# Performance work log

Measured on AMD Instinct MI355X. Metric: run time of the kernel, lower is better.

The kernel has to match this reference:

```python
import jax, jax.numpy as jnp
import numpy as np

N_EMBD = 1024
N_HEAD = 16
HEAD_DIM = N_EMBD // N_HEAD


def setup_inputs() -> dict:
    key = jax.random.key(0)
    ks = jax.random.split(key, 5)
    B, T, C = 4, 2048, N_EMBD
    x = jax.random.normal(ks[0], (B, T, C), dtype=jnp.float32)
    # torch Linear: y = x @ W.T + b; store W in [out, in] like torch
    scale = 1.0 / np.sqrt(C)
    W_attn = jax.random.normal(ks[1], (3 * C, C), dtype=jnp.float32) * scale
    b_attn = jnp.zeros((3 * C,), dtype=jnp.float32)
    W_proj = jax.random.normal(ks[2], (C, C), dtype=jnp.float32) * scale
    b_proj = jnp.zeros((C,), dtype=jnp.float32)
    return {"x": x, "W_attn": W_attn, "b_attn": b_attn, "W_proj": W_proj, "b_proj": b_proj}


def reference(x, W_attn, b_attn, W_proj, b_proj):
    B, T, C = x.shape
    H, D = N_HEAD, HEAD_DIM
    qkv = x @ W_attn.T + b_attn                    # [B,T,3C]
    q, k, v = jnp.split(qkv, 3, axis=-1)
    q = q.reshape(B, T, H, D).transpose(0, 2, 1, 3)  # [B,H,T,D]
    k = k.reshape(B, T, H, D).transpose(0, 2, 1, 3)
    v = v.reshape(B, T, H, D).transpose(0, 2, 1, 3)
    att = jnp.einsum('bhtd,bhsd->bhts', q, k) / jnp.sqrt(jnp.float32(D))  # [B,H,T,T]
    causal = jnp.tril(jnp.ones((T, T), dtype=bool))
    att = jnp.where(causal[None, None], att, -jnp.inf)
    att = jax.nn.softmax(att, axis=-1)
    # dropout is identity in eval mode (pdrop=0.0)
    y = jnp.einsum('bhts,bhsd->bhtd', att, v)      # [B,H,T,D]
    y = y.transpose(0, 2, 1, 3).reshape(B, T, C)
    return y @ W_proj.T + b_proj
```

## Files before the change

### kernel.cpp

```cpp
#include <hip/hip_runtime.h>
#include <stdint.h>


#define SEQ 2048
#define NBATCH 4
#define CEMB 1024
#define NHEAD 16
#define DHEAD 64
#define BTROWS (NBATCH * SEQ)

typedef __bf16 bf16x8 __attribute__((ext_vector_type(8)));
typedef float f32x4 __attribute__((ext_vector_type(4)));
typedef float f32x16 __attribute__((ext_vector_type(16)));
typedef uint32_t u32x4 __attribute__((ext_vector_type(4)));
typedef unsigned short u16;

__device__ __forceinline__ u16 f2bf(float f) {
  union { float f; uint32_t u; } x; x.f = f;
  uint32_t u = x.u;
  return (u16)((u + 0x7FFFu + ((u >> 16) & 1u)) >> 16);
}

__device__ __forceinline__ uint32_t pk2(float a, float b) {
  union { __bf16 h[2]; uint32_t u; } z;
  z.h[0] = (__bf16)a; z.h[1] = (__bf16)b;
  return z.u;
}

__device__ __forceinline__ void gload_lds16(const void* g, void* l) {
  __builtin_amdgcn_global_load_lds(
      (const __attribute__((address_space(1))) uint32_t*)g,
      (__attribute__((address_space(3))) uint32_t*)l, 16, 0, 0);
}

__global__ __launch_bounds__(256) void cvt_f32_bf16_kernel(
    const float* __restrict__ in, u16* __restrict__ out, int n4) {
  int i = blockIdx.x * blockDim.x + threadIdx.x;
  int stride = gridDim.x * blockDim.x;
  for (; i < n4; i += stride) {
    float4 v = reinterpret_cast<const float4*>(in)[i];
    ushort4 o;
    o.x = f2bf(v.x); o.y = f2bf(v.y); o.z = f2bf(v.z); o.w = f2bf(v.w);
    reinterpret_cast<ushort4*>(out)[i] = o;
  }
}

template <bool OUT_BF16>
__global__ __launch_bounds__(256) void gemm_bt_kernel(
    const u16* __restrict__ A, const u16* __restrict__ Bt,
    const float* __restrict__ bias, void* __restrict__ Cout,
    int M, int N, int K) {
  __shared__ u16 As[128][64];
  __shared__ u16 Bs[128][64];
  const int tid = threadIdx.x;
  const int lane = tid & 63;
  const int wave = tid >> 6;
  const int wr = wave >> 1, wc = wave & 1;
  const int m0 = blockIdx.y * 128;
  const int n0 = blockIdx.x * 128;
  const int l15 = lane & 15, lhi = lane >> 4;

  f32x4 acc[4][4];
#pragma unroll
  for (int i = 0; i < 4; i++)
#pragma unroll
    for (int j = 0; j < 4; j++) acc[i][j] = (f32x4){0.f, 0.f, 0.f, 0.f};

  const int srow = lane >> 3;
  const int scol = (lane & 7) * 8;

  for (int kt = 0; kt < K; kt += 64) {
#pragma unroll
    for (int i = 0; i < 4; i++) {
      int rr = (wave * 4 + i) * 8 + srow;
      gload_lds16(A + (size_t)(m0 + rr) * K + kt + scol, &As[(wave * 4 + i) * 8][0]);
      gload_lds16(Bt + (size_t)(n0 + rr) * K + kt + scol, &Bs[(wave * 4 + i) * 8][0]);
    }
    __syncthreads();
#pragma unroll
    for (int ks = 0; ks < 2; ks++) {
      bf16x8 af[4], bfr[4];
#pragma unroll
      for (int mi = 0; mi < 4; mi++)
        af[mi] = *(const bf16x8*)&As[wr * 64 + mi * 16 + l15][ks * 32 + lhi * 8];
#pragma unroll
      for (int ni = 0; ni < 4; ni++)
        bfr[ni] = *(const bf16x8*)&Bs[wc * 64 + ni * 16 + l15][ks * 32 + lhi * 8];
#pragma unroll
      for (int mi = 0; mi < 4; mi++)
#pragma unroll
        for (int ni = 0; ni < 4; ni++)
          acc[mi][ni] = __builtin_amdgcn_mfma_f32_16x16x32_bf16(
              af[mi], bfr[ni], acc[mi][ni], 0, 0, 0);
    }
    __syncthreads();
  }

#pragma unroll
  for (int mi = 0; mi < 4; mi++) {
#pragma unroll
    for (int ni = 0; ni < 4; ni++) {
      int n = n0 + wc * 64 + ni * 16 + l15;
      float bv = bias[n];
#pragma unroll
      for (int r = 0; r < 4; r++) {
        int m = m0 + wr * 64 + mi * 16 + lhi * 4 + r;
        float v = acc[mi][ni][r] + bv;
        if constexpr (OUT_BF16)
          ((u16*)Cout)[(size_t)m * N + n] = f2bf(v);
        else
          ((float*)Cout)[(size_t)m * N + n] = v;
      }
    }
  }
}

__global__ __launch_bounds__(256) void attn_kernel(
    const u16* __restrict__ qkv, u16* __restrict__ yatt) {
  __shared__ u16 Ks[64][64];
  __shared__ u16 Vt[64][68];

  const int tid = threadIdx.x;
  const int lane = tid & 63;
  const int wave = tid >> 6;
  const int qt = 15 - (int)blockIdx.x;
  const int bh = blockIdx.y;
  const int b = bh >> 4, h = bh & 15;
  const int l31 = lane & 31, hi = lane >> 5;

  const size_t rs = 3 * CEMB;
  const u16* qb = qkv + (size_t)b * SEQ * rs + h * DHEAD;
  const u16* kb = qb + CEMB;
  const u16* vb = qb + 2 * CEMB;

  const int q0 = qt * 128;
  const int qabs = q0 + wave * 32 + l31;

  bf16x8 qf[4];
  {
    const u16* qp = qb + (size_t)qabs * rs + hi * 8;
#pragma unroll
    for (int dc = 0; dc < 4; dc++) qf[dc] = *(const bf16x8*)(qp + dc * 16);
  }

  float m_acc = -1e30f, l_acc = 0.f;
  f32x16 o_acc[2];
  o_acc[0] = (f32x16)(0.f);
  o_acc[1] = (f32x16)(0.f);

  const float SCLL2E = 0.125f * 1.44269504088896f;

  for (int s0 = 0; s0 <= q0 + 64; s0 += 64) {
#pragma unroll
    for (int c = 0; c < 2; c++) {
      int row0 = (c * 4 + wave) * 8;
      int row = row0 + (lane >> 3);
      int cb = (lane & 7) ^ (row & 7);
      gload_lds16(kb + (size_t)(s0 + row) * rs + cb * 8, &Ks[row0][0]);
    }
    {
      const u16* gv = vb + (size_t)(s0 + lane) * rs + wave * 16;
      union { u32x4 q[2]; u16 u[16]; } tv;
      tv.q[0] = *(const u32x4*)gv;
      tv.q[1] = *(const u32x4*)(gv + 8);
#pragma unroll
      for (int j = 0; j < 16; j++) Vt[wave * 16 + j][lane] = tv.u[j];
    }
    __syncthreads();

    const bool active = (s0 <= q0 + wave * 32 + 31);
    if (active) {
      f32x16 sf[2];
#pragma unroll
      for (int kt = 0; kt < 2; kt++) {
        f32x16 s = (f32x16)(0.f);
        int key = kt * 32 + l31;
#pragma unroll
        for (int dc = 0; dc < 4; dc++) {
          int cb = (dc * 2 + hi) ^ (key & 7);
          const bf16x8 kf = *(const bf16x8*)((const u16*)&Ks[key][0] + cb * 8);
          s = __builtin_amdgcn_mfma_f32_32x32x16_bf16(kf, qf[dc], s, 0, 0, 0);
        }
        sf[kt] = s;
      }

      if (s0 + 63 > q0 + wave * 32) {
#pragma unroll
        for (int kt = 0; kt < 2; kt++)
#pragma unroll
          for (int r = 0; r < 16; r++) {
            int key = s0 + kt * 32 + (r & 3) + 8 * (r >> 2) + 4 * hi;
            if (key > qabs) sf[kt][r] = -3e38f;
          }
      }

      float cmax = sf[0][0];
#pragma unroll
      for (int r = 1; r < 16; r++) cmax = fmaxf(cmax, sf[0][r]);
#pragma unroll
      for (int r = 0; r < 16; r++) cmax = fmaxf(cmax, sf[1][r]);
      cmax = fmaxf(cmax, __shfl_xor(cmax, 32, 64));

      if (!__all(cmax <= m_acc + 64.0f)) {
        float mnew = fmaxf(m_acc, cmax);
        float scf = __builtin_amdgcn_exp2f((m_acc - mnew) * SCLL2E);
        m_acc = mnew;
        l_acc *= scf;
        float scr[16];
#pragma unroll
        for (int r = 0; r < 16; r++)
          scr[r] = __shfl(scf, (r & 3) + 8 * (r >> 2) + 4 * hi, 64);
#pragma unroll
        for (int r = 0; r < 16; r++) {
          o_acc[0][r] *= scr[r];
          o_acc[1][r] *= scr[r];
        }
      }

      const float c1 = -m_acc * SCLL2E;
      float ps = 0.f;
#pragma unroll
      for (int kt = 0; kt < 2; kt++)
#pragma unroll
        for (int r = 0; r < 16; r++) {
          float p = __builtin_amdgcn_exp2f(fmaf(sf[kt][r], SCLL2E, c1));
          sf[kt][r] = p;
          ps += p;
        }
      ps += __shfl_xor(ps, 32, 64);
      l_acc += ps;

      bf16x8 pa[4];
#pragma unroll
      for (int ks = 0; ks < 4; ks++) {
        const int t = ks >> 1;
        const int ra = (ks & 1) * 8;
        uint32_t a  = pk2(sf[t][ra + 0], sf[t][ra + 1]);
        uint32_t b2 = pk2(sf[t][ra + 2], sf[t][ra + 3]);
        uint32_t cc = pk2(sf[t][ra + 4], sf[t][ra + 5]);
        uint32_t dd = pk2(sf[t][ra + 6], sf[t][ra + 7]);
        uint32_t snd0 = hi ? a : cc;
        uint32_t snd1 = hi ? b2 : dd;
        uint32_t r0 = __shfl_xor(snd0, 32, 64);
        uint32_t r1 = __shfl_xor(snd1, 32, 64);
        union { bf16x8 v; uint32_t w[4]; } u;
        u.w[0] = hi ? r0 : a;
        u.w[1] = hi ? r1 : b2;
        u.w[2] = hi ? cc : r0;
        u.w[3] = hi ? dd : r1;
        pa[ks] = u.v;
      }

#pragma unroll
      for (int dt = 0; dt < 2; dt++) {
        const u16* vrow = &Vt[dt * 32 + l31][hi * 8];
#pragma unroll
        for (int ks = 0; ks < 4; ks++) {
          union { bf16x8 v; uint2 d[2]; } u;
          u.d[0] = *(const uint2*)(vrow + ks * 16);
          u.d[1] = *(const uint2*)(vrow + ks * 16 + 4);
          o_acc[dt] = __builtin_amdgcn_mfma_f32_32x32x16_bf16(pa[ks], u.v, o_acc[dt], 0, 0, 0);
        }
      }
    }
    __syncthreads();
  }

  float rl = 1.0f / l_acc;
#pragma unroll
  for (int r = 0; r < 16; r++) {
    int crow = (r & 3) + 8 * (r >> 2) + 4 * hi;
    float linv = __shfl(rl, crow, 64);
    int t = q0 + wave * 32 + crow;
    u16* yp = yatt + ((size_t)(b * SEQ + t)) * CEMB + h * DHEAD + l31;
    yp[0]  = f2bf(o_acc[0][r] * linv);
    yp[32] = f2bf(o_acc[1][r] * linv);
  }
}

extern "C" void kernel_launch(void* const* d_in, const int* in_sizes, int n_in,
                              void* d_out, int out_size, void* d_ws, size_t ws_size,
                              hipStream_t stream) {
  const float* x      = (const float*)d_in[0];
  const float* W_attn = (const float*)d_in[1];
  const float* b_attn = (const float*)d_in[2];
  const float* W_proj = (const float*)d_in[3];
  const float* b_proj = (const float*)d_in[4];
  float* out = (float*)d_out;

  u16* Xb   = (u16*)d_ws;
  u16* Wab  = Xb  + (size_t)BTROWS * CEMB;
  u16* Wpb  = Wab + (size_t)3 * CEMB * CEMB;
  u16* QKV  = Wpb + (size_t)CEMB * CEMB;
  u16* Yatt = QKV + (size_t)BTROWS * 3 * CEMB;

  cvt_f32_bf16_kernel<<<2048, 256, 0, stream>>>(x, Xb, BTROWS * CEMB / 4);
  cvt_f32_bf16_kernel<<<1024, 256, 0, stream>>>(W_attn, Wab, 3 * CEMB * CEMB / 4);
  cvt_f32_bf16_kernel<<<512, 256, 0, stream>>>(W_proj, Wpb, CEMB * CEMB / 4);

  gemm_bt_kernel<true><<<dim3(3 * CEMB / 128, BTROWS / 128), 256, 0, stream>>>(
      Xb, Wab, b_attn, QKV, BTROWS, 3 * CEMB, CEMB);

  attn_kernel<<<dim3(SEQ / 128, NBATCH * NHEAD), 256, 0, stream>>>(QKV, Yatt);

  gemm_bt_kernel<false><<<dim3(CEMB / 128, BTROWS / 128), 256, 0, stream>>>(
      Yatt, Wpb, b_proj, out, BTROWS, CEMB, CEMB);
}
```

Baseline: 339.1 us.

## Pair causal query tiles per block and widen attention key tiles to 128

Each attention block now handles two query tiles, p and 15-p, one after the other. This balances the causal workload across blocks and halves the grid. The key/value tile grows from 64 to 128 keys per iteration, which halves the barrier count and lets the masking apply only to the diagonal tile. It also adds s_setprio around the MFMA sections and tree reductions for the row max and sum. The cost is more LDS and registers per block and fewer blocks in flight, which could hurt occupancy.

Result: faster. 331.1 us (-2.4%).

```diff
diff --git a/kernel.cpp b/kernel.cpp
--- a/kernel.cpp
+++ b/kernel.cpp
@@ -117,13 +117,13 @@
 
 __global__ __launch_bounds__(256) void attn_kernel(
     const u16* __restrict__ qkv, u16* __restrict__ yatt) {
-  __shared__ u16 Ks[64][64];
-  __shared__ u16 Vt[64][68];
+  __shared__ u16 Ks[128][64];
+  __shared__ u16 Vt[64][132];
 
   const int tid = threadIdx.x;
   const int lane = tid & 63;
   const int wave = tid >> 6;
-  const int qt = 15 - (int)blockIdx.x;
+  const int p = blockIdx.x;
   const int bh = blockIdx.y;
   const int b = bh >> 4, h = bh & 15;
   const int l31 = lane & 31, hi = lane >> 5;
@@ -133,46 +133,48 @@
   const u16* kb = qb + CEMB;
   const u16* vb = qb + 2 * CEMB;
 
-  const int q0 = qt * 128;
-  const int qabs = q0 + wave * 32 + l31;
-
-  bf16x8 qf[4];
-  {
-    const u16* qp = qb + (size_t)qabs * rs + hi * 8;
-#pragma unroll
-    for (int dc = 0; dc < 4; dc++) qf[dc] = *(const bf16x8*)(qp + dc * 16);
-  }
-
-  float m_acc = -1e30f, l_acc = 0.f;
-  f32x16 o_acc[2];
-  o_acc[0] = (f32x16)(0.f);
-  o_acc[1] = (f32x16)(0.f);
-
   const float SCLL2E = 0.125f * 1.44269504088896f;
 
-  for (int s0 = 0; s0 <= q0 + 64; s0 += 64) {
-#pragma unroll
-    for (int c = 0; c < 2; c++) {
-      int row0 = (c * 4 + wave) * 8;
-      int row = row0 + (lane >> 3);
-      int cb = (lane & 7) ^ (row & 7);
-      gload_lds16(kb + (size_t)(s0 + row) * rs + cb * 8, &Ks[row0][0]);
-    }
+  for (int pass = 0; pass < 2; ++pass) {
+    const int qt = pass ? (15 - p) : p;
+    const int q0 = qt * 128;
+    const int qabs = q0 + wave * 32 + l31;
+
+    bf16x8 qf[4];
     {
-      const u16* gv = vb + (size_t)(s0 + lane) * rs + wave * 16;
-      union { u32x4 q[2]; u16 u[16]; } tv;
-      tv.q[0] = *(const u32x4*)gv;
-      tv.q[1] = *(const u32x4*)(gv + 8);
-#pragma unroll
-      for (int j = 0; j < 16; j++) Vt[wave * 16 + j][lane] = tv.u[j];
-    }
-    __syncthreads();
-
-    const bool active = (s0 <= q0 + wave * 32 + 31);
-    if (active) {
-      f32x16 sf[2];
-#pragma unroll
-      for (int kt = 0; kt < 2; kt++) {
+      const u16* qp = qb + (size_t)qabs * rs + hi * 8;
+#pragma unroll
+      for (int dc = 0; dc < 4; dc++) qf[dc] = *(const bf16x8*)(qp + dc * 16);
+    }
+
+    float m_acc = -1e30f, l_acc = 0.f;
+    f32x16 o_acc[2];
+    o_acc[0] = (f32x16)(0.f);
+    o_acc[1] = (f32x16)(0.f);
+
+    for (int s0 = 0; s0 <= q0; s0 += 128) {
+#pragma unroll
+      for (int c = 0; c < 4; c++) {
+        int row0 = (c * 4 + wave) * 8;
+        int row = row0 + (lane >> 3);
+        int cb = (lane & 7) ^ (row & 7);
+        gload_lds16(kb + (size_t)(s0 + row) * rs + cb * 8, &Ks[row0][0]);
+      }
+#pragma unroll
+      for (int half = 0; half < 2; ++half) {
+        const u16* gv = vb + (size_t)(s0 + half * 64 + lane) * rs + wave * 16;
+        union { u32x4 q[2]; u16 u[16]; } tv;
+        tv.q[0] = *(const u32x4*)gv;
+        tv.q[1] = *(const u32x4*)(gv + 8);
+#pragma unroll
+        for (int j = 0; j < 16; j++) Vt[wave * 16 + j][half * 64 + lane] = tv.u[j];
+      }
+      __syncthreads();
+
+      f32x16 sf[4];
+      __builtin_amdgcn_s_setprio(1);
+#pragma unroll
+      for (int kt = 0; kt < 4; kt++) {
         f32x16 s = (f32x16)(0.f);
         int key = kt * 32 + l31;
 #pragma unroll
@@ -183,10 +185,11 @@
         }
         sf[kt] = s;
       }
-
-      if (s0 + 63 > q0 + wave * 32) {
-#pragma unroll
-        for (int kt = 0; kt < 2; kt++)
+      __builtin_amdgcn_s_setprio(0);
+
+      if (s0 == q0) {
+#pragma unroll
+        for (int kt = 0; kt < 4; kt++)
 #pragma unroll
           for (int r = 0; r < 16; r++) {
             int key = s0 + kt * 32 + (r & 3) + 8 * (r >> 2) + 4 * hi;
@@ -194,11 +197,15 @@
           }
       }
 
-      float cmax = sf[0][0];
-#pragma unroll
-      for (int r = 1; r < 16; r++) cmax = fmaxf(cmax, sf[0][r]);
-#pragma unroll
-      for (int r = 0; r < 16; r++) cmax = fmaxf(cmax, sf[1][r]);
+      float t16[16];
+#pragma unroll
+      for (int i = 0; i < 16; i++)
+        t16[i] = fmaxf(fmaxf(sf[0][i], sf[1][i]), fmaxf(sf[2][i], sf[3][i]));
+#pragma unroll
+      for (int i = 0; i < 8; i++) t16[i] = fmaxf(t16[i], t16[i + 8]);
+#pragma unroll
+      for (int i = 0; i < 4; i++) t16[i] = fmaxf(t16[i], t16[i + 4]);
+      float cmax = fmaxf(fmaxf(t16[0], t16[1]), fmaxf(t16[2], t16[3]));
       cmax = fmaxf(cmax, __shfl_xor(cmax, 32, 64));
 
       if (!__all(cmax <= m_acc + 64.0f)) {
@@ -218,21 +225,25 @@
       }
 
       const float c1 = -m_acc * SCLL2E;
-      float ps = 0.f;
-#pragma unroll
-      for (int kt = 0; kt < 2; kt++)
-#pragma unroll
-        for (int r = 0; r < 16; r++) {
-          float p = __builtin_amdgcn_exp2f(fmaf(sf[kt][r], SCLL2E, c1));
-          sf[kt][r] = p;
-          ps += p;
-        }
+#pragma unroll
+      for (int kt = 0; kt < 4; kt++)
+#pragma unroll
+        for (int r = 0; r < 16; r++)
+          sf[kt][r] = __builtin_amdgcn_exp2f(fmaf(sf[kt][r], SCLL2E, c1));
+#pragma unroll
+      for (int i = 0; i < 16; i++)
+        t16[i] = (sf[0][i] + sf[1][i]) + (sf[2][i] + sf[3][i]);
+#pragma unroll
+      for (int i = 0; i < 8; i++) t16[i] = t16[i] + t16[i + 8];
+#pragma unroll
+      for (int i = 0; i < 4; i++) t16[i] = t16[i] + t16[i + 4];
+      float ps = (t16[0] + t16[1]) + (t16[2] + t16[3]);
       ps += __shfl_xor(ps, 32, 64);
       l_acc += ps;
 
-      bf16x8 pa[4];
-#pragma unroll
-      for (int ks = 0; ks < 4; ks++) {
+      bf16x8 pa[8];
+#pragma unroll
+      for (int ks = 0; ks < 8; ks++) {
         const int t = ks >> 1;
         const int ra = (ks & 1) * 8;
         uint32_t a  = pk2(sf[t][ra + 0], sf[t][ra + 1]);
@@ -251,30 +262,32 @@
         pa[ks] = u.v;
       }
 
+      __builtin_amdgcn_s_setprio(1);
 #pragma unroll
       for (int dt = 0; dt < 2; dt++) {
         const u16* vrow = &Vt[dt * 32 + l31][hi * 8];
 #pragma unroll
-        for (int ks = 0; ks < 4; ks++) {
+        for (int ks = 0; ks < 8; ks++) {
           union { bf16x8 v; uint2 d[2]; } u;
           u.d[0] = *(const uint2*)(vrow + ks * 16);
           u.d[1] = *(const uint2*)(vrow + ks * 16 + 4);
           o_acc[dt] = __builtin_amdgcn_mfma_f32_32x32x16_bf16(pa[ks], u.v, o_acc[dt], 0, 0, 0);
         }
       }
-    }
-    __syncthreads();
-  }
-
-  float rl = 1.0f / l_acc;
-#pragma unroll
-  for (int r = 0; r < 16; r++) {
-    int crow = (r & 3) + 8 * (r >> 2) + 4 * hi;
-    float linv = __shfl(rl, crow, 64);
-    int t = q0 + wave * 32 + crow;
-    u16* yp = yatt + ((size_t)(b * SEQ + t)) * CEMB + h * DHEAD + l31;
-    yp[0]  = f2bf(o_acc[0][r] * linv);
-    yp[32] = f2bf(o_acc[1][r] * linv);
+      __builtin_amdgcn_s_setprio(0);
+      __syncthreads();
+    }
+
+    float rl = 1.0f / l_acc;
+#pragma unroll
+    for (int r = 0; r < 16; r++) {
+      int crow = (r & 3) + 8 * (r >> 2) + 4 * hi;
+      float linv = __shfl(rl, crow, 64);
+      int t = q0 + wave * 32 + crow;
+      u16* yp = yatt + ((size_t)(b * SEQ + t)) * CEMB + h * DHEAD + l31;
+      yp[0]  = f2bf(o_acc[0][r] * linv);
+      yp[32] = f2bf(o_acc[1][r] * linv);
+    }
   }
 }
 
@@ -301,7 +314,7 @@
   gemm_bt_kernel<true><<<dim3(3 * CEMB / 128, BTROWS / 128), 256, 0, stream>>>(
       Xb, Wab, b_attn, QKV, BTROWS, 3 * CEMB, CEMB);
 
-  attn_kernel<<<dim3(SEQ / 128, NBATCH * NHEAD), 256, 0, stream>>>(QKV, Yatt);
+  attn_kernel<<<dim3(8, NBATCH * NHEAD), 256, 0, stream>>>(QKV, Yatt);
 
   gemm_bt_kernel<false><<<dim3(CEMB / 128, BTROWS / 128), 256, 0, stream>>>(
       Yatt, Wpb, b_proj, out, BTROWS, CEMB, CEMB);
```
